# Kernel optimization log

Measured on AMD Instinct MI355X. Metric: run time of the kernel, lower is better.

Reference implementation:

```python
import jax, jax.numpy as jnp
import numpy as np

N = 100000
E = 1600000
F_IN = 128
H = 256
C = 40
BN_EPS = 1e-5


def setup_inputs() -> dict:
    key = jax.random.key(0)
    ks = jax.random.split(key, 16)
    x = jax.random.normal(ks[0], (N, F_IN), dtype=jnp.float32)
    edge_index = jax.random.randint(ks[1], (2, E), 0, N, dtype=jnp.int64)
    # pre layer
    pre_w = jax.random.normal(ks[2], (H, F_IN), dtype=jnp.float32) * (1.0 / np.sqrt(F_IN))
    pre_b = jnp.zeros((H,), jnp.float32)
    # batchnorm params stacked [5, 4, H]: gamma, beta, running_mean, running_var
    gamma = jnp.ones((5, H), jnp.float32)
    beta = jnp.zeros((5, H), jnp.float32)
    rmean = jax.random.normal(ks[3], (5, H), dtype=jnp.float32) * 0.1
    rvar = jax.random.uniform(ks[4], (5, H), dtype=jnp.float32) * 0.5 + 0.5
    bn_params = jnp.stack([gamma, beta, rmean, rvar], axis=1)  # [5,4,H]
    # 3 SAGEConv layers: lin_l (neighbor, with bias), lin_r (root, no bias)
    s = 1.0 / np.sqrt(H)
    lin_l_w = jax.random.normal(ks[5], (3, H, H), dtype=jnp.float32) * s
    lin_l_b = jnp.zeros((3, H), jnp.float32)
    lin_r_w = jax.random.normal(ks[6], (3, H, H), dtype=jnp.float32) * s
    # post layers
    post1_w = jax.random.normal(ks[7], (H, H), dtype=jnp.float32) * s
    post1_b = jnp.zeros((H,), jnp.float32)
    post2_w = jax.random.normal(ks[8], (C, H), dtype=jnp.float32) * s
    post2_b = jnp.zeros((C,), jnp.float32)
    return {
        "x": x, "edge_index": edge_index,
        "pre_w": pre_w, "pre_b": pre_b, "bn_params": bn_params,
        "lin_l_w": lin_l_w, "lin_l_b": lin_l_b, "lin_r_w": lin_r_w,
        "post1_w": post1_w, "post1_b": post1_b,
        "post2_w": post2_w, "post2_b": post2_b,
    }


def _bn(x, p):
    # eval-mode BatchNorm1d with running stats; p: [4, H]
    g, b, m, v = p[0], p[1], p[2], p[3]
    return (x - m) * (g * jax.lax.rsqrt(v + BN_EPS)) + b


def _sage_conv(x, src, dst, wl, bl, wr):
    # PyG SAGEConv (aggr='mean'): lin_l(mean_{j in N(i)} x_j) + lin_r(x_i)
    msg = x[src]                                             # [E, H] gather
    agg = jax.ops.segment_sum(msg, dst, num_segments=N)       # [N, H] scatter
    cnt = jax.ops.segment_sum(jnp.ones((src.shape[0],), x.dtype), dst, num_segments=N)
    mean = agg / jnp.maximum(cnt, 1.0)[:, None]
    return mean @ wl.T + bl + x @ wr.T


def reference(x, edge_index, pre_w, pre_b, bn_params, lin_l_w, lin_l_b, lin_r_w,
              post1_w, post1_b, post2_w, post2_b):
    src, dst = edge_index[0], edge_index[1]
    h = x @ pre_w.T + pre_b
    h = jax.nn.relu(_bn(h, bn_params[0]))  # dropout is identity in eval mode
    for i in range(3):
        h = _sage_conv(h, src, dst, lin_l_w[i], lin_l_b[i], lin_r_w[i])
        h = jax.nn.relu(_bn(h, bn_params[i + 1]))
    h = h @ post1_w.T + post1_b
    h = jax.nn.relu(_bn(h, bn_params[4]))
    logits = h @ post2_w.T + post2_b
    return jax.nn.log_softmax(logits, axis=1)
```

## Files before the change

kernel.cpp:

```cpp
#include <hip/hip_runtime.h>
#include <cstdint>
#include <cstddef>

#define N_NODES 100000
#define N_EDGES 1600000
#define F_INDIM 128
#define HDIM 256
#define C_OUT 40
#define BN_EPS 1e-5f

typedef unsigned short bf16_t;
typedef __attribute__((ext_vector_type(8))) short bf16x8;
typedef __attribute__((ext_vector_type(4))) float f32x4;

__device__ __forceinline__ float bf2f(unsigned int u) {
  return __uint_as_float(u << 16);
}
__device__ __forceinline__ bf16_t f2bf(float f) {
  unsigned int x = __float_as_uint(f);
  return (bf16_t)((x + 0x7fffu + ((x >> 16) & 1u)) >> 16);
}

__global__ void k_cvt(const float* __restrict__ s, bf16_t* __restrict__ d, int n) {
  int i = (blockIdx.x * blockDim.x + threadIdx.x) * 4;
  if (i >= n) return;
  float4 v = *reinterpret_cast<const float4*>(&s[i]);
  uint2 o;
  o.x = (unsigned)f2bf(v.x) | ((unsigned)f2bf(v.y) << 16);
  o.y = (unsigned)f2bf(v.z) | ((unsigned)f2bf(v.w) << 16);
  *reinterpret_cast<uint2*>(&d[i]) = o;
}

__global__ void k_rank(const int* __restrict__ dst, int* __restrict__ cursor,
                       int* __restrict__ rank, int E) {
  for (int e = blockIdx.x * blockDim.x + threadIdx.x; e < E; e += gridDim.x * blockDim.x)
    rank[e] = atomicAdd(&cursor[dst[e]], 1);
}

__global__ __launch_bounds__(1024)
void k_scan_local(const int* __restrict__ cnt, int* __restrict__ row_ptr,
                  int* __restrict__ blk_sum, int n) {
  __shared__ int buf[1024];
  int tid = threadIdx.x;
  int i = blockIdx.x * 1024 + tid;
  int v = (i < n) ? cnt[i] : 0;
  buf[tid] = v;
  __syncthreads();
  for (int off = 1; off < 1024; off <<= 1) {
    int t = (tid >= off) ? buf[tid - off] : 0;
    __syncthreads();
    buf[tid] += t;
    __syncthreads();
  }
  if (i < n) row_ptr[i] = buf[tid] - v;
  if (tid == 1023) blk_sum[blockIdx.x] = buf[1023];
}

__global__ __launch_bounds__(128)
void k_scan_blk(const int* __restrict__ blk_sum, int* __restrict__ blk_off, int nb) {
  __shared__ int buf[128];
  int tid = threadIdx.x;
  int v = (tid < nb) ? blk_sum[tid] : 0;
  buf[tid] = v;
  __syncthreads();
  for (int off = 1; off < 128; off <<= 1) {
    int t = (tid >= off) ? buf[tid - off] : 0;
    __syncthreads();
    buf[tid] += t;
    __syncthreads();
  }
  if (tid < nb) blk_off[tid] = buf[tid] - v;
}

__global__ void k_scan_add(int* __restrict__ row_ptr, const int* __restrict__ blk_off, int n) {
  int i = blockIdx.x * blockDim.x + threadIdx.x;
  if (i < n) row_ptr[i] += blk_off[i >> 10];
  if (i == 0) row_ptr[n] = N_EDGES;
}

__global__ void k_place(const int* __restrict__ src, const int* __restrict__ dst,
                        const int* __restrict__ rank, const int* __restrict__ row_ptr,
                        int* __restrict__ csr, int E) {
  for (int e = blockIdx.x * blockDim.x + threadIdx.x; e < E; e += gridDim.x * blockDim.x)
    csr[row_ptr[dst[e]] + rank[e]] = src[e];
}

__global__ void k_inv(const int* __restrict__ cnt, float* __restrict__ inv, int n) {
  int i = blockIdx.x * blockDim.x + threadIdx.x;
  if (i < n) inv[i] = 1.0f / (float)(cnt[i] > 0 ? cnt[i] : 1);
}

__device__ __forceinline__ void add8(float* acc, uint4 r) {
  acc[0] += bf2f(r.x & 0xffffu); acc[1] += bf2f(r.x >> 16);
  acc[2] += bf2f(r.y & 0xffffu); acc[3] += bf2f(r.y >> 16);
  acc[4] += bf2f(r.z & 0xffffu); acc[5] += bf2f(r.z >> 16);
  acc[6] += bf2f(r.w & 0xffffu); acc[7] += bf2f(r.w >> 16);
}

__global__ __launch_bounds__(256)
void k_aggregate(const bf16_t* __restrict__ h, const int* __restrict__ row_ptr,
                 const int* __restrict__ csr, const float* __restrict__ inv_deg,
                 bf16_t* __restrict__ mean) {
  int w = threadIdx.x >> 6, lane = threadIdx.x & 63;
  int node = blockIdx.x * 4 + w;
  if (node >= N_NODES) return;
  int beg = row_ptr[node], end = row_ptr[node + 1];
  int half = lane >> 5;
  int l32 = lane & 31;
  float acc[8] = {};
  int deg = end - beg;
  int p = beg;
  int p8 = beg + (deg & ~7);
  for (; p < p8; p += 8) {
    int s0 = csr[p + half];
    int s1 = csr[p + 2 + half];
    int s2 = csr[p + 4 + half];
    int s3 = csr[p + 6 + half];
    uint4 r0 = *reinterpret_cast<const uint4*>(&h[(size_t)s0 * HDIM + l32 * 8]);
    uint4 r1 = *reinterpret_cast<const uint4*>(&h[(size_t)s1 * HDIM + l32 * 8]);
    uint4 r2 = *reinterpret_cast<const uint4*>(&h[(size_t)s2 * HDIM + l32 * 8]);
    uint4 r3 = *reinterpret_cast<const uint4*>(&h[(size_t)s3 * HDIM + l32 * 8]);
    add8(acc, r0);
    add8(acc, r1);
    add8(acc, r2);
    add8(acc, r3);
  }
  if (end - p >= 4) {
    int s0 = csr[p + half];
    int s1 = csr[p + 2 + half];
    uint4 r0 = *reinterpret_cast<const uint4*>(&h[(size_t)s0 * HDIM + l32 * 8]);
    uint4 r1 = *reinterpret_cast<const uint4*>(&h[(size_t)s1 * HDIM + l32 * 8]);
    add8(acc, r0);
    add8(acc, r1);
    p += 4;
  }
  for (; p < end; p += 2) {
    int e = p + half;
    if (e < end) {
      int s = csr[e];
      uint4 r = *reinterpret_cast<const uint4*>(&h[(size_t)s * HDIM + l32 * 8]);
      add8(acc, r);
    }
  }
#pragma unroll
  for (int k = 0; k < 8; ++k) acc[k] += __shfl_xor(acc[k], 32);
  if (half == 0) {
    float iv = inv_deg[node];
    uint4 o;
    o.x = (unsigned)f2bf(acc[0] * iv) | ((unsigned)f2bf(acc[1] * iv) << 16);
    o.y = (unsigned)f2bf(acc[2] * iv) | ((unsigned)f2bf(acc[3] * iv) << 16);
    o.z = (unsigned)f2bf(acc[4] * iv) | ((unsigned)f2bf(acc[5] * iv) << 16);
    o.w = (unsigned)f2bf(acc[6] * iv) | ((unsigned)f2bf(acc[7] * iv) << 16);
    *reinterpret_cast<uint4*>(&mean[(size_t)node * HDIM + l32 * 8]) = o;
  }
}

__device__ __forceinline__ void store1(float* p, float v) { *p = v; }
__device__ __forceinline__ void store1(bf16_t* p, float v) { *p = f2bf(v); }

#define LDSK 40

template <typename TOUT>
__global__ __launch_bounds__(256)
void gemm_mfma(const bf16_t* __restrict__ A0, const bf16_t* __restrict__ W0,
               const bf16_t* __restrict__ A1, const bf16_t* __restrict__ W1,
               const float* __restrict__ bias, const float* __restrict__ bn,
               TOUT* __restrict__ C, int M, int K, int OUT, int dual) {
  __shared__ bf16_t lds[2][(128 + 128) * LDSK];
  const int tid = threadIdx.x;
  const int lane = tid & 63, wid = tid >> 6;
  const int wm = wid >> 1, wn = wid & 1;
  const int row0 = blockIdx.x * 128, col0 = blockIdx.y * 128;
  const int l15 = lane & 15, l4 = lane >> 4;

  const int srow = tid >> 1;
  const int sk = (tid & 1) * 16;

  const int nk = K / 32;
  const int nsteps = dual ? nk * 2 : nk;

  f32x4 acc[4][4] = {};
  uint4 va0, va1, vb0, vb1;

  auto stage_load = [&](int s) {
    const bf16_t* A = (s < nk) ? A0 : A1;
    const bf16_t* W = (s < nk) ? W0 : W1;
    int kk = ((s < nk) ? s : s - nk) * 32 + sk;
    uint4 z; z.x = z.y = z.z = z.w = 0u;
    va0 = z; va1 = z; vb0 = z; vb1 = z;
    int ar = row0 + srow;
    if (ar < M) {
      const uint4* p = reinterpret_cast<const uint4*>(&A[(size_t)ar * K + kk]);
      va0 = p[0]; va1 = p[1];
    }
    int br = col0 + srow;
    if (br < OUT) {
      const uint4* p = reinterpret_cast<const uint4*>(&W[(size_t)br * K + kk]);
      vb0 = p[0]; vb1 = p[1];
    }
  };
  auto stage_write = [&](int b) {
    uint4* la = reinterpret_cast<uint4*>(&lds[b][srow * LDSK + sk]);
    la[0] = va0; la[1] = va1;
    uint4* lb = reinterpret_cast<uint4*>(&lds[b][(128 + srow) * LDSK + sk]);
    lb[0] = vb0; lb[1] = vb1;
  };

  stage_load(0);
  stage_write(0);
  __syncthreads();
  int cur = 0;
  for (int s = 0; s < nsteps; ++s) {
    if (s + 1 < nsteps) stage_load(s + 1);
    const bf16_t* pa = &lds[cur][(wm * 64 + l15) * LDSK + l4 * 8];
    const bf16_t* pb = &lds[cur][(128 + wn * 64 + l15) * LDSK + l4 * 8];
    bf16x8 a[4], b[4];
#pragma unroll
    for (int i = 0; i < 4; ++i) a[i] = *reinterpret_cast<const bf16x8*>(&pa[i * 16 * LDSK]);
#pragma unroll
    for (int j = 0; j < 4; ++j) b[j] = *reinterpret_cast<const bf16x8*>(&pb[j * 16 * LDSK]);
#pragma unroll
    for (int i = 0; i < 4; ++i)
#pragma unroll
      for (int j = 0; j < 4; ++j)
        acc[i][j] = __builtin_amdgcn_mfma_f32_16x16x32_bf16(a[i], b[j], acc[i][j], 0, 0, 0);
    if (s + 1 < nsteps) {
      stage_write(cur ^ 1);
      __syncthreads();
      cur ^= 1;
    }
  }

#pragma unroll
  for (int j = 0; j < 4; ++j) {
    int col = col0 + wn * 64 + j * 16 + l15;
    if (col >= OUT) continue;
    float bs = bias ? bias[col] : 0.f;
    float scale = 1.f, shift = bs;
    bool has_bn = (bn != nullptr);
    if (has_bn) {
      float g = bn[col], bb = bn[256 + col], mm = bn[512 + col], vv = bn[768 + col];
      float is = g * rsqrtf(vv + BN_EPS);
      scale = is; shift = (bs - mm) * is + bb;
    }
#pragma unroll
    for (int i = 0; i < 4; ++i) {
#pragma unroll
      for (int r = 0; r < 4; ++r) {
        int row = row0 + wm * 64 + i * 16 + l4 * 4 + r;
        if (row >= M) continue;
        float v = acc[i][j][r];
        v = has_bn ? fmaxf(v * scale + shift, 0.f) : (v + bs);
        store1(&C[(size_t)row * OUT + col], v);
      }
    }
  }
}

__global__ __launch_bounds__(256)
void k_logsoftmax(const float* __restrict__ logits, float* __restrict__ out, int M) {
  int row = blockIdx.x * 4 + (threadIdx.x >> 6);
  if (row >= M) return;
  int lane = threadIdx.x & 63;
  float v = (lane < C_OUT) ? logits[(size_t)row * C_OUT + lane] : -1e30f;
  float m = v;
#pragma unroll
  for (int o = 32; o; o >>= 1) m = fmaxf(m, __shfl_xor(m, o));
  float e = (lane < C_OUT) ? expf(v - m) : 0.f;
  float s = e;
#pragma unroll
  for (int o = 32; o; o >>= 1) s += __shfl_xor(s, o);
  if (lane < C_OUT) out[(size_t)row * C_OUT + lane] = v - m - logf(s);
}

extern "C" void kernel_launch(void* const* d_in, const int* in_sizes, int n_in,
                              void* d_out, int out_size, void* d_ws, size_t ws_size,
                              hipStream_t stream) {
  const float* x       = (const float*)d_in[0];
  const int*   ei      = (const int*)d_in[1];
  const float* pre_w   = (const float*)d_in[2];
  const float* pre_b   = (const float*)d_in[3];
  const float* bn      = (const float*)d_in[4];
  const float* lin_l_w = (const float*)d_in[5];
  const float* lin_l_b = (const float*)d_in[6];
  const float* lin_r_w = (const float*)d_in[7];
  const float* post1_w = (const float*)d_in[8];
  const float* post1_b = (const float*)d_in[9];
  const float* post2_w = (const float*)d_in[10];
  const float* post2_b = (const float*)d_in[11];
  float* out = (float*)d_out;

  const int* src = ei;
  const int* dstv = ei + N_EDGES;

  char* base = (char*)d_ws;
  size_t off = 0;
  auto alloc = [&](size_t bytes) -> void* {
    void* p = base + off;
    off = (off + bytes + 255) & ~(size_t)255;
    return p;
  };
  bf16_t* hA = (bf16_t*)alloc((size_t)N_NODES * HDIM * 2);
  bf16_t* hB = (bf16_t*)alloc((size_t)N_NODES * HDIM * 2);
  bf16_t* hC = (bf16_t*)alloc((size_t)N_NODES * HDIM * 2);
  int* row_ptr = (int*)alloc((size_t)(N_NODES + 1) * 4);
  int* cursor  = (int*)alloc((size_t)N_NODES * 4);
  int* csr     = (int*)alloc((size_t)N_EDGES * 4);
  int* rank    = (int*)alloc((size_t)N_EDGES * 4);
  float* inv   = (float*)alloc((size_t)N_NODES * 4);
  int* blk_sum = (int*)alloc(128 * 4);
  int* blk_off = (int*)alloc(128 * 4);
  bf16_t* w_pre = (bf16_t*)alloc((size_t)HDIM * F_INDIM * 2);
  bf16_t* w_ll  = (bf16_t*)alloc((size_t)3 * HDIM * HDIM * 2);
  bf16_t* w_lr  = (bf16_t*)alloc((size_t)3 * HDIM * HDIM * 2);
  bf16_t* w_p1  = (bf16_t*)alloc((size_t)HDIM * HDIM * 2);
  bf16_t* w_p2  = (bf16_t*)alloc((size_t)C_OUT * HDIM * 2);
  (void)n_in; (void)in_sizes; (void)out_size;
  if (off > ws_size) return;

  bf16_t* x_bf = hB;

  {
    int n;
    n = N_NODES * F_INDIM;
    k_cvt<<<(n / 4 + 255) / 256, 256, 0, stream>>>(x, x_bf, n);
    n = HDIM * F_INDIM;
    k_cvt<<<(n / 4 + 255) / 256, 256, 0, stream>>>(pre_w, w_pre, n);
    n = 3 * HDIM * HDIM;
    k_cvt<<<(n / 4 + 255) / 256, 256, 0, stream>>>(lin_l_w, w_ll, n);
    k_cvt<<<(n / 4 + 255) / 256, 256, 0, stream>>>(lin_r_w, w_lr, n);
    n = HDIM * HDIM;
    k_cvt<<<(n / 4 + 255) / 256, 256, 0, stream>>>(post1_w, w_p1, n);
    n = C_OUT * HDIM;
    k_cvt<<<(n / 4 + 255) / 256, 256, 0, stream>>>(post2_w, w_p2, n);
  }

  hipMemsetAsync(cursor, 0, (size_t)N_NODES * 4, stream);
  k_rank<<<2048, 256, 0, stream>>>(dstv, cursor, rank, N_EDGES);
  int nb = (N_NODES + 1023) / 1024;
  k_scan_local<<<nb, 1024, 0, stream>>>(cursor, row_ptr, blk_sum, N_NODES);
  k_scan_blk<<<1, 128, 0, stream>>>(blk_sum, blk_off, nb);
  k_scan_add<<<(N_NODES + 255) / 256, 256, 0, stream>>>(row_ptr, blk_off, N_NODES);
  k_place<<<2048, 256, 0, stream>>>(src, dstv, rank, row_ptr, csr, N_EDGES);
  k_inv<<<(N_NODES + 255) / 256, 256, 0, stream>>>(cursor, inv, N_NODES);

  dim3 gH((N_NODES + 127) / 128, 2);
  gemm_mfma<bf16_t><<<gH, 256, 0, stream>>>(
      x_bf, w_pre, nullptr, nullptr, pre_b, bn, hA, N_NODES, F_INDIM, HDIM, 0);

  bf16_t* hcur = hA;
  bf16_t* hnext = hC;
  for (int i = 0; i < 3; ++i) {
    k_aggregate<<<N_NODES / 4, 256, 0, stream>>>(hcur, row_ptr, csr, inv, hB);
    gemm_mfma<bf16_t><<<gH, 256, 0, stream>>>(
        hB, w_ll + (size_t)i * HDIM * HDIM,
        hcur, w_lr + (size_t)i * HDIM * HDIM,
        lin_l_b + (size_t)i * HDIM,
        bn + (size_t)(i + 1) * 4 * HDIM,
        hnext, N_NODES, HDIM, HDIM, 1);
    bf16_t* t = hcur; hcur = hnext; hnext = t;
  }
  gemm_mfma<bf16_t><<<gH, 256, 0, stream>>>(
      hcur, w_p1, nullptr, nullptr, post1_b,
      bn + (size_t)4 * 4 * HDIM, hnext, N_NODES, HDIM, HDIM, 0);
  float* logits = (float*)hB;
  dim3 gC((N_NODES + 127) / 128, 1);
  gemm_mfma<float><<<gC, 256, 0, stream>>>(
      hnext, w_p2, nullptr, nullptr, post2_b,
      nullptr, logits, N_NODES, HDIM, C_OUT, 0);
  k_logsoftmax<<<(N_NODES + 3) / 4, 256, 0, stream>>>(logits, out, N_NODES);
}
```

Baseline: 813.4 us.

## Use direct global-to-LDS loads in MFMA GEMM staging

Replaces the register-staged global loads plus LDS writes in the bf16 MFMA GEMM with global_load_lds builtins that copy 16 bytes per lane straight into shared memory. The LDS layout changes from padded rows (stride 40) to unpadded 32-wide rows, and out-of-range rows are clamped instead of zero-filled. The aim is to cut VGPR pressure and the separate LDS store instructions. The trade-off is possible LDS bank conflicts on the unpadded layout. There is also a correctness risk: no explicit vmcnt wait before the barrier, and the prefetch into the other buffer is issued while that buffer may still be read.

```diff
diff --git a/kernel.cpp b/kernel.cpp
--- a/kernel.cpp
+++ b/kernel.cpp
@@ -158,74 +158,70 @@
 __device__ __forceinline__ void store1(float* p, float v) { *p = v; }
 __device__ __forceinline__ void store1(bf16_t* p, float v) { *p = f2bf(v); }
 
-#define LDSK 40
-
 template <typename TOUT>
 __global__ __launch_bounds__(256)
 void gemm_mfma(const bf16_t* __restrict__ A0, const bf16_t* __restrict__ W0,
                const bf16_t* __restrict__ A1, const bf16_t* __restrict__ W1,
                const float* __restrict__ bias, const float* __restrict__ bn,
                TOUT* __restrict__ C, int M, int K, int OUT, int dual) {
-  __shared__ bf16_t lds[2][(128 + 128) * LDSK];
+  __shared__ bf16_t lds[2][2][128 * 32];
   const int tid = threadIdx.x;
   const int lane = tid & 63, wid = tid >> 6;
   const int wm = wid >> 1, wn = wid & 1;
   const int row0 = blockIdx.x * 128, col0 = blockIdx.y * 128;
   const int l15 = lane & 15, l4 = lane >> 4;
 
-  const int srow = tid >> 1;
-  const int sk = (tid & 1) * 16;
-
   const int nk = K / 32;
   const int nsteps = dual ? nk * 2 : nk;
 
   f32x4 acc[4][4] = {};
-  uint4 va0, va1, vb0, vb1;
-
-  auto stage_load = [&](int s) {
+
+  const int srow_base = wid * 32 + (lane >> 2);
+  const int skk = (lane & 3) * 8;
+
+  auto stage = [&](int s, int b) {
     const bf16_t* A = (s < nk) ? A0 : A1;
     const bf16_t* W = (s < nk) ? W0 : W1;
-    int kk = ((s < nk) ? s : s - nk) * 32 + sk;
-    uint4 z; z.x = z.y = z.z = z.w = 0u;
-    va0 = z; va1 = z; vb0 = z; vb1 = z;
-    int ar = row0 + srow;
-    if (ar < M) {
-      const uint4* p = reinterpret_cast<const uint4*>(&A[(size_t)ar * K + kk]);
-      va0 = p[0]; va1 = p[1];
-    }
-    int br = col0 + srow;
-    if (br < OUT) {
-      const uint4* p = reinterpret_cast<const uint4*>(&W[(size_t)br * K + kk]);
-      vb0 = p[0]; vb1 = p[1];
+    int kk0 = ((s < nk) ? s : s - nk) * 32 + skk;
+#pragma unroll
+    for (int c = 0; c < 2; ++c) {
+      int chunk = wid * 2 + c;
+      int row = srow_base + c * 16;
+      int ar = row0 + row; if (ar >= M) ar = M - 1;
+      int br = col0 + row; if (br >= OUT) br = OUT - 1;
+      const bf16_t* gA = &A[(size_t)ar * K + kk0];
+      const bf16_t* gB = &W[(size_t)br * K + kk0];
+      __builtin_amdgcn_global_load_lds(
+          (const __attribute__((address_space(1))) unsigned int*)gA,
+          (__attribute__((address_space(3))) unsigned int*)&lds[b][0][chunk * 512],
+          16, 0, 0);
+      __builtin_amdgcn_global_load_lds(
+          (const __attribute__((address_space(1))) unsigned int*)gB,
+          (__attribute__((address_space(3))) unsigned int*)&lds[b][1][chunk * 512],
+          16, 0, 0);
     }
   };
-  auto stage_write = [&](int b) {
-    uint4* la = reinterpret_cast<uint4*>(&lds[b][srow * LDSK + sk]);
-    la[0] = va0; la[1] = va1;
-    uint4* lb = reinterpret_cast<uint4*>(&lds[b][(128 + srow) * LDSK + sk]);
-    lb[0] = vb0; lb[1] = vb1;
-  };
-
-  stage_load(0);
-  stage_write(0);
+
+  stage(0, 0);
   __syncthreads();
   int cur = 0;
   for (int s = 0; s < nsteps; ++s) {
-    if (s + 1 < nsteps) stage_load(s + 1);
-    const bf16_t* pa = &lds[cur][(wm * 64 + l15) * LDSK + l4 * 8];
-    const bf16_t* pb = &lds[cur][(128 + wn * 64 + l15) * LDSK + l4 * 8];
+    if (s + 1 < nsteps) stage(s + 1, cur ^ 1);
+    const bf16_t* pa = &lds[cur][0][l15 * 32 + l4 * 8];
+    const bf16_t* pb = &lds[cur][1][l15 * 32 + l4 * 8];
     bf16x8 a[4], b[4];
 #pragma unroll
-    for (int i = 0; i < 4; ++i) a[i] = *reinterpret_cast<const bf16x8*>(&pa[i * 16 * LDSK]);
-#pragma unroll
-    for (int j = 0; j < 4; ++j) b[j] = *reinterpret_cast<const bf16x8*>(&pb[j * 16 * LDSK]);
+    for (int i = 0; i < 4; ++i)
+      a[i] = *reinterpret_cast<const bf16x8*>(&pa[(wm * 64 + i * 16) * 32]);
+#pragma unroll
+    for (int j = 0; j < 4; ++j)
+      b[j] = *reinterpret_cast<const bf16x8*>(&pb[(wn * 64 + j * 16) * 32]);
 #pragma unroll
     for (int i = 0; i < 4; ++i)
 #pragma unroll
       for (int j = 0; j < 4; ++j)
         acc[i][j] = __builtin_amdgcn_mfma_f32_16x16x32_bf16(a[i], b[j], acc[i][j], 0, 0, 0);
     if (s + 1 < nsteps) {
-      stage_write(cur ^ 1);
       __syncthreads();
       cur ^= 1;
     }
```

Result: faster. 794.0 us (-2.4%).
